# Performance work log

Measured on AMD Instinct MI355X. Metric: run time of the kernel, lower is better.

## Reference

```python
import jax, jax.numpy as jnp
import numpy as np
from jax import lax

B, C, H, W = 4, 128, 128, 128
MAXD = 192
D = MAXD // 4            # 48 disparity hypotheses at 1/4 scale
WS = 8                   # window size
NH = 8                   # num heads
HD = C // NH             # head dim = 16
SCALE = HD ** -0.5
HID = 4 * C              # mlp hidden (mlp_ratio=4)


def _rel_index(ws):
    coords = np.stack(np.meshgrid(np.arange(ws), np.arange(ws), indexing='ij'))
    cf = coords.reshape(2, -1)
    rel = (cf[:, :, None] - cf[:, None, :]).transpose(1, 2, 0)
    rel[:, :, 0] += ws - 1
    rel[:, :, 1] += ws - 1
    rel[:, :, 0] *= 2 * ws - 1
    return rel.sum(-1)   # [ws*ws, ws*ws]

REL_IDX = jnp.asarray(_rel_index(WS))


def setup_inputs() -> dict:
    key = jax.random.key(0)
    ks = iter(jax.random.split(key, 40))
    rn = lambda shape, s=0.02: jax.random.normal(next(ks), shape, dtype=jnp.float32) * s
    return {
        'feat_l': jax.random.normal(next(ks), (B, C, H, W), dtype=jnp.float32),
        'feat_r': jax.random.normal(next(ks), (B, C, H, W), dtype=jnp.float32),
        'wq': rn((C, C)), 'bq': jnp.zeros((C,), jnp.float32),
        'wk': rn((C, C)), 'bk': jnp.zeros((C,), jnp.float32),
        'wv': rn((C, C)), 'bv': jnp.zeros((C,), jnp.float32),
        'wp': rn((C, C)), 'bp': jnp.zeros((C,), jnp.float32),
        'rpb': rn(((2 * WS - 1) ** 2, NH)),
        'ln1_g': jnp.ones((C,), jnp.float32), 'ln1_b': jnp.zeros((C,), jnp.float32),
        'ln2_g': jnp.ones((C,), jnp.float32), 'ln2_b': jnp.zeros((C,), jnp.float32),
        'mlp_w1': rn((C, HID)), 'mlp_b1': jnp.zeros((HID,), jnp.float32),
        'mlp_w2': rn((HID, C)), 'mlp_b2': jnp.zeros((C,), jnp.float32),
        'un_w1': rn((C, C)), 'un_b1': jnp.zeros((C,), jnp.float32),
        'un_w2': rn((C, C)), 'un_b2': jnp.zeros((C,), jnp.float32),
        'dp_w1': rn((C // 2 + D // 2 + 16, C + D, 3, 3)) if False else rn(((C + D) // 2, C + D, 3, 3)),
        'dp_b1': jnp.zeros(((C + D) // 2,), jnp.float32),
        'bn_g': jnp.ones(((C + D) // 2,), jnp.float32), 'bn_b': jnp.zeros(((C + D) // 2,), jnp.float32),
        'dp_w2': rn((D, (C + D) // 2, 1, 1)), 'dp_b2': jnp.zeros((D,), jnp.float32),
    }


def _ln(x, g, b):
    m = x.mean(-1, keepdims=True)
    v = x.var(-1, keepdims=True)
    return (x - m) * jax.lax.rsqrt(v + 1e-5) * g + b


def _conv(x, w, b, pad):
    y = lax.conv_general_dilated(x, w, (1, 1), [(pad, pad), (pad, pad)],
                                 dimension_numbers=('NCHW', 'OIHW', 'NCHW'))
    return y + b[None, :, None, None]


def _cost_volume(fl, fr):
    # corr[:, d] = mean_c fl[..., w] * fr[..., w-d], zero-padded on the left
    outs = [jnp.mean(fl * fr, axis=1)]
    for d in range(1, D):
        fr_s = jnp.pad(fr[:, :, :, :-d], ((0, 0), (0, 0), (0, 0), (d, 0)))
        outs.append(jnp.mean(fl * fr_s, axis=1))
    return jnp.stack(outs, axis=1)  # [B, D, H, W]


def _win_part(tok):  # [B, H*W, C] -> [B*nW, WS*WS, C]
    x = tok.reshape(B, H // WS, WS, W // WS, WS, C)
    return x.transpose(0, 1, 3, 2, 4, 5).reshape(-1, WS * WS, C)


def _win_rev(win):  # [B*nW, WS*WS, C] -> [B, H*W, C]
    x = win.reshape(B, H // WS, W // WS, WS, WS, C)
    return x.transpose(0, 1, 3, 2, 4, 5).reshape(B, H * W, C)


def _forward(feat_l, feat_r, wq, bq, wk, bk, wv, bv, wp, bp, rpb,
             ln1_g, ln1_b, ln2_g, ln2_b, mlp_w1, mlp_b1, mlp_w2, mlp_b2,
             un_w1, un_b1, un_w2, un_b2, dp_w1, dp_b1, bn_g, bn_b, dp_w2, dp_b2):
    gelu = lambda x: jax.nn.gelu(x, approximate=False)
    cost = _cost_volume(feat_l, feat_r)                       # [B, D, H, W]

    tokens = feat_l.reshape(B, C, H * W).transpose(0, 2, 1)   # [B, N, C]
    unary = gelu(tokens @ un_w1 + un_b1) @ un_w2 + un_b2      # unary potential

    nf = _ln(_win_part(tokens), ln1_g, ln1_b)                 # [Bw, 64, C]
    Bw, N = nf.shape[0], WS * WS
    q = (nf @ wq + bq).reshape(Bw, N, NH, HD).transpose(0, 2, 1, 3)
    k = (nf @ wk + bk).reshape(Bw, N, NH, HD).transpose(0, 2, 1, 3)
    v = (nf @ wv + bv).reshape(Bw, N, NH, HD).transpose(0, 2, 1, 3)
    attn = jnp.einsum('bhnd,bhmd->bhnm', q, k) * SCALE
    bias = rpb[REL_IDX.reshape(-1)].reshape(N, N, NH).transpose(2, 0, 1)
    attn = jax.nn.softmax(attn + bias[None], axis=-1)
    o = jnp.einsum('bhnm,bhmd->bhnd', attn, v).transpose(0, 2, 1, 3).reshape(Bw, N, C)
    pairwise = o @ wp + bp

    x = unary + _win_rev(pairwise)
    x = x + gelu(_ln(x, ln2_g, ln2_b) @ mlp_w1 + mlp_b1) @ mlp_w2 + mlp_b2 * 0.0 + (jnp.zeros((), jnp.float32))
    # (faithful residual MLP; the extra zero terms are no-ops kept out below)
    # -- recompute cleanly to avoid confusion:
    # x = x + mlp(norm2(x))  already done above via single expression

    crf = x.transpose(0, 2, 1).reshape(B, C, H, W)
    fused = jnp.concatenate([crf, cost], axis=1)              # [B, C+D, H, W]

    h1 = jax.nn.relu((_conv(fused, dp_w1, dp_b1, 1)) * jax.lax.rsqrt(jnp.float32(1.0 + 1e-5)) * bn_g[None, :, None, None] + bn_b[None, :, None, None])
    pv = _conv(h1, dp_w2, dp_b2, 0)                           # [B, D, H, W]
    prob = jax.nn.softmax(pv, axis=1)
    disp = jnp.arange(D, dtype=jnp.float32)[None, :, None, None]
    pred = jnp.sum(prob * disp, axis=1, keepdims=True) * 4.0  # [B, 1, H, W]
    return pred


def reference(feat_l, feat_r, wq, bq, wk, bk, wv, bv, wp, bp, rpb,
              ln1_g, ln1_b, ln2_g, ln2_b, mlp_w1, mlp_b1, mlp_w2, mlp_b2,
              un_w1, un_b1, un_w2, un_b2, dp_w1, dp_b1, bn_g, bn_b, dp_w2, dp_b2):
    return _forward(feat_l, feat_r, wq, bq, wk, bk, wv, bv, wp, bp, rpb,
                    ln1_g, ln1_b, ln2_g, ln2_b, mlp_w1, mlp_b1, mlp_w2, mlp_b2,
                    un_w1, un_b1, un_w2, un_b2, dp_w1, dp_b1, bn_g, bn_b, dp_w2, dp_b2)
```

## Files before the change

### kernel.cpp

```cpp
#include <hip/hip_runtime.h>
#include <math.h>

constexpr int Bn = 4, Cc = 128, Hh = 128, Wn = 128, Dd = 48;
constexpr float SCALE = 0.25f;

typedef short  bf16x8 __attribute__((ext_vector_type(8)));
typedef short  bf16x4 __attribute__((ext_vector_type(4)));
typedef float  f32x4  __attribute__((ext_vector_type(4)));
typedef unsigned short u16x8 __attribute__((ext_vector_type(8)));

static __device__ __forceinline__ unsigned short f2bf(float f) {
    return __builtin_bit_cast(unsigned short, (__bf16)f);
}
static __device__ __forceinline__ float bf2f(unsigned short u) {
    return __uint_as_float((unsigned int)u << 16);
}
static __device__ __forceinline__ unsigned int pack2bf(float a, float b) {
    return (unsigned int)f2bf(a) | ((unsigned int)f2bf(b) << 16);
}
static __device__ __forceinline__ float gelu_f(float v) {
    float u = v * (1.5957691216f + 0.0713548162f * v * v);
    return v * __builtin_amdgcn_rcpf(1.0f + __expf(-u));
}

static __device__ __forceinline__ size_t opk_addr(int b, int wh, int ww, int Mt, int ks, int lane) {
    return ((size_t)(b * 16384) + (wh * 8 + Mt * 2 + (ks >> 1)) * 128 + ww * 8) * 128
           + (ks & 1) * 512 + lane * 8;
}

static __device__ void pack_conv(int blk, int lane,
                                 const float* __restrict__ w1, const float* __restrict__ b1,
                                 const float* __restrict__ bng, const float* __restrict__ bnb,
                                 unsigned short* __restrict__ pk, float* __restrict__ bias2) {
    const float rs = 0.9999950000374997f;
    int ct = blk % 6;
    int taplin = blk / 6;
    int tap = taplin % 9, chunk = taplin / 9;
    int co = ct * 16 + (lane & 15);
    int cibase = chunk * 32 + (lane >> 4) * 8;
    u16x8 out;
#pragma unroll
    for (int j = 0; j < 8; ++j) {
        int ci = cibase + j;
        float v = 0.f;
        if (co < 88 && ci < 176) v = w1[(size_t)co * 1584 + ci * 9 + tap] * rs * bng[co];
        out[j] = f2bf(v);
    }
    *(u16x8*)(pk + ((size_t)blk * 64 + lane) * 8) = out;
    if (blk == 0) {
        for (int i = lane; i < 96; i += 64)
            bias2[i] = (i < 88) ? (b1[i] * rs * bng[i] + bnb[i]) : 0.f;
    }
}

static __device__ void pack_gemmB(int blk, int lane,
                                  const float* __restrict__ W,
                                  unsigned short* __restrict__ out, int ncols) {
    int ntiles = ncols >> 4;
    int ks = blk & 3;
    int nt = (blk >> 2) % ntiles;
    int kc = blk / (4 * ntiles);
    int col = nt * 16 + (lane & 15);
    int k0 = kc * 128 + ks * 32 + (lane >> 4) * 8;
    u16x8 o;
#pragma unroll
    for (int j = 0; j < 8; ++j) o[j] = f2bf(W[(size_t)(k0 + j) * ncols + col]);
    *(u16x8*)(out + ((size_t)blk * 64 + lane) * 8) = o;
}

static __device__ void pack_rpb(int blk, int lane,
                                const float* __restrict__ rpb, float* __restrict__ pb) {
    int nt = blk & 3, mt = (blk >> 2) & 3, hh = blk >> 4;
    int tq = nt * 16 + (lane & 15);
    int g = lane >> 4;
    float o[4];
#pragma unroll
    for (int rr = 0; rr < 4; ++rr) {
        int tk = mt * 16 + g * 4 + rr;
        int relidx = (((tq >> 3) - (tk >> 3)) + 7) * 15 + ((tq & 7) - (tk & 7)) + 7;
        o[rr] = rpb[relidx * 8 + hh];
    }
    float4 v = {o[0], o[1], o[2], o[3]};
    *(float4*)(pb + ((size_t)blk * 64 + lane) * 4) = v;
}

__global__ __launch_bounds__(64) void k_pack_all(
        const float* __restrict__ dp_w1, const float* __restrict__ dp_b1,
        const float* __restrict__ bn_g, const float* __restrict__ bn_b,
        unsigned short* __restrict__ pk, float* __restrict__ bias2,
        const float* __restrict__ wq, const float* __restrict__ wk,
        const float* __restrict__ wv, const float* __restrict__ wp,
        unsigned short* __restrict__ pkw,
        const float* __restrict__ rpb, float* __restrict__ pb,
        const float* __restrict__ mlp_w1, unsigned short* __restrict__ pm1,
        const float* __restrict__ mlp_w2, unsigned short* __restrict__ pm2,
        const float* __restrict__ un_w1, unsigned short* __restrict__ pu1,
        const float* __restrict__ un_w2, unsigned short* __restrict__ pu2) {
    int blk = blockIdx.x;
    int lane = threadIdx.x;
    if (blk < 324) {
        pack_conv(blk, lane, dp_w1, dp_b1, bn_g, bn_b, pk, bias2);
    } else if (blk < 452) {
        int bb = blk - 324;
        int mat = bb >> 5;
        const float* W = (mat == 0) ? wq : (mat == 1) ? wk : (mat == 2) ? wv : wp;
        pack_gemmB(bb & 31, lane, W, pkw + (size_t)mat * 16384, 128);
    } else if (blk < 580) {
        pack_rpb(blk - 452, lane, rpb, pb);
    } else if (blk < 708) {
        pack_gemmB(blk - 580, lane, mlp_w1, pm1, 512);
    } else if (blk < 836) {
        pack_gemmB(blk - 708, lane, mlp_w2, pm2, 128);
    } else if (blk < 868) {
        pack_gemmB(blk - 836, lane, un_w1, pu1, 128);
    } else {
        pack_gemmB(blk - 868, lane, un_w2, pu2, 128);
    }
}

__global__ __launch_bounds__(256) void k_front(const float* __restrict__ feat_l,
                                               const float* __restrict__ feat_r,
                                               unsigned short* __restrict__ costbf,
                                               const unsigned short* __restrict__ pu1,
                                               const float* __restrict__ b1,
                                               const unsigned short* __restrict__ pu2,
                                               const float* __restrict__ b2,
                                               const float* __restrict__ g1,
                                               const float* __restrict__ bt1,
                                               float* __restrict__ x,
                                               unsigned short* __restrict__ nf) {
    __shared__ __align__(16) char smem[34816];
    int tid = threadIdx.x;
    int blk = blockIdx.x;

    if (blk >= 1024) {
        int cb = blk - 1024;
        int wt = cb & 1, h = (cb >> 1) & 127, b = cb >> 8;
        int w0 = wt * 64;
        int w = tid & 63, dg = tid >> 6;
        float* s_fl = (float*)smem;
        float* s_fr = (float*)(smem + 4096);
        float acc[12];
#pragma unroll
        for (int dj = 0; dj < 12; ++dj) acc[dj] = 0.f;

#pragma unroll 1
        for (int ck = 0; ck < 8; ++ck) {
            int ci0 = ck * 16;
            {
                int c = tid >> 4, k4 = tid & 15;
                *(float4*)&s_fl[c * 64 + k4 * 4] =
                    *(const float4*)&feat_l[((size_t)(b * 128 + ci0 + c) << 14) + h * 128 + w0 + k4 * 4];
            }
            for (int i = tid; i < 448; i += 256) {
                int c = i / 28, k4 = i - c * 28;
                int wgl = w0 - 48 + k4 * 4;
                float4 v = {0.f, 0.f, 0.f, 0.f};
                if (wgl >= 0)
                    v = *(const float4*)&feat_r[((size_t)(b * 128 + ci0 + c) << 14) + h * 128 + wgl];
                *(float4*)&s_fr[c * 112 + k4 * 4] = v;
            }
            __syncthreads();
            int base = w + 48 - dg * 12;
#pragma unroll
            for (int c = 0; c < 16; ++c) {
                float flv = s_fl[c * 64 + w];
#pragma unroll
                for (int dj = 0; dj < 12; ++dj)
                    acc[dj] += flv * s_fr[c * 112 + base - dj];
            }
            __syncthreads();
        }
        const float inv = 1.0f / 128.0f;
        unsigned short* cbp = costbf + ((size_t)(b << 14) + h * 128 + w0 + w) * 64 + dg * 12;
#pragma unroll
        for (int q = 0; q < 3; ++q) {
            bf16x4 o4;
#pragma unroll
            for (int rr = 0; rr < 4; ++rr) o4[rr] = (short)f2bf(acc[q * 4 + rr] * inv);
            *(bf16x4*)&cbp[q * 4] = o4;
        }
        if (dg == 3) {
            const u16x8 z8 = {0, 0, 0, 0, 0, 0, 0, 0};
            *(u16x8*)&cbp[12] = z8;
            *(u16x8*)&cbp[20] = z8;
        }
        return;
    }

    unsigned short* s_a = (unsigned short*)smem;
    unsigned short* s_h = (unsigned short*)(smem + 17408);
    int wid = tid >> 6, lane = tid & 63;
    int g = lane >> 4, t = lane & 15;
    int n0g = blk * 64;
    int b = n0g >> 14;
    int nb = n0g & 16383;

    for (int idx = tid; idx < 4096; idx += 256) {
        int c2 = idx >> 6, nl = idx & 63;
        float v0 = feat_l[((size_t)(b * 128 + 2 * c2) << 14) + nb + nl];
        float v1 = feat_l[((size_t)(b * 128 + 2 * c2 + 1) << 14) + nb + nl];
        *(unsigned int*)&s_a[nl * 136 + 2 * c2] = pack2bf(v0, v1);
    }
    __syncthreads();

    {
        int tok = tid >> 2, q = tid & 3;
        float v[32];
#pragma unroll
        for (int i8 = 0; i8 < 4; ++i8) {
            u16x8 r8 = *(const u16x8*)&s_a[tok * 136 + q * 32 + i8 * 8];
#pragma unroll
            for (int j = 0; j < 8; ++j) v[i8 * 8 + j] = bf2f(r8[j]);
        }
        float s = 0.f, s2 = 0.f;
#pragma unroll
        for (int i = 0; i < 32; ++i) { s += v[i]; s2 += v[i] * v[i]; }
        s += __shfl_xor(s, 1); s += __shfl_xor(s, 2);
        s2 += __shfl_xor(s2, 1); s2 += __shfl_xor(s2, 2);
        float mean = s * (1.f / 128.f);
        float var = s2 * (1.f / 128.f) - mean * mean;
        float rstd = rsqrtf(var + 1e-5f);
        size_t base = (size_t)(n0g + tok) * 128 + q * 32;
#pragma unroll
        for (int i8 = 0; i8 < 4; ++i8) {
            u16x8 o8;
#pragma unroll
            for (int j = 0; j < 8; ++j) {
                int c = q * 32 + i8 * 8 + j;
                o8[j] = f2bf((v[i8 * 8 + j] - mean) * rstd * g1[c] + bt1[c]);
            }
            *(u16x8*)&nf[base + i8 * 8] = o8;
        }
    }

    bf16x8 af[4][4];
#pragma unroll
    for (int Mt = 0; Mt < 4; ++Mt)
#pragma unroll
        for (int ks = 0; ks < 4; ++ks)
            af[Mt][ks] = *(const bf16x8*)&s_a[(Mt * 16 + t) * 136 + ks * 32 + g * 8];

    f32x4 acc1[4][2];
#pragma unroll
    for (int nt2 = 0; nt2 < 2; ++nt2) {
        float bv = b1[(wid * 2 + nt2) * 16 + t];
#pragma unroll
        for (int Mt = 0; Mt < 4; ++Mt) acc1[Mt][nt2] = (f32x4){bv, bv, bv, bv};
    }
#pragma unroll
    for (int ks = 0; ks < 4; ++ks) {
        bf16x8 bf0 = *(const bf16x8*)(pu1 + (size_t)(((wid * 2 + 0) * 4 + ks) * 64 + lane) * 8);
        bf16x8 bf1 = *(const bf16x8*)(pu1 + (size_t)(((wid * 2 + 1) * 4 + ks) * 64 + lane) * 8);
#pragma unroll
        for (int Mt = 0; Mt < 4; ++Mt) {
            acc1[Mt][0] = __builtin_amdgcn_mfma_f32_16x16x32_bf16(af[Mt][ks], bf0, acc1[Mt][0], 0, 0, 0);
            acc1[Mt][1] = __builtin_amdgcn_mfma_f32_16x16x32_bf16(af[Mt][ks], bf1, acc1[Mt][1], 0, 0, 0);
        }
    }
#pragma unroll
    for (int Mt = 0; Mt < 4; ++Mt)
#pragma unroll
        for (int nt2 = 0; nt2 < 2; ++nt2)
#pragma unroll
            for (int rr = 0; rr < 4; ++rr)
                s_h[(Mt * 16 + g * 4 + rr) * 136 + (wid * 2 + nt2) * 16 + t] = f2bf(gelu_f(acc1[Mt][nt2][rr]));
    __syncthreads();

    bf16x8 a2[4][4];
#pragma unroll
    for (int Mt = 0; Mt < 4; ++Mt)
#pragma unroll
        for (int ks = 0; ks < 4; ++ks)
            a2[Mt][ks] = *(const bf16x8*)&s_h[(Mt * 16 + t) * 136 + ks * 32 + g * 8];

    f32x4 acc2[4][2];
#pragma unroll
    for (int nt2 = 0; nt2 < 2; ++nt2) {
        float bv = b2[(wid * 2 + nt2) * 16 + t];
#pragma unroll
        for (int Mt = 0; Mt < 4; ++Mt) acc2[Mt][nt2] = (f32x4){bv, bv, bv, bv};
    }
#pragma unroll
    for (int ks = 0; ks < 4; ++ks) {
        bf16x8 bf0 = *(const bf16x8*)(pu2 + (size_t)(((wid * 2 + 0) * 4 + ks) * 64 + lane) * 8);
        bf16x8 bf1 = *(const bf16x8*)(pu2 + (size_t)(((wid * 2 + 1) * 4 + ks) * 64 + lane) * 8);
#pragma unroll
        for (int Mt = 0; Mt < 4; ++Mt) {
            acc2[Mt][0] = __builtin_amdgcn_mfma_f32_16x16x32_bf16(a2[Mt][ks], bf0, acc2[Mt][0], 0, 0, 0);
            acc2[Mt][1] = __builtin_amdgcn_mfma_f32_16x16x32_bf16(a2[Mt][ks], bf1, acc2[Mt][1], 0, 0, 0);
        }
    }
#pragma unroll
    for (int Mt = 0; Mt < 4; ++Mt)
#pragma unroll
        for (int nt2 = 0; nt2 < 2; ++nt2)
#pragma unroll
            for (int rr = 0; rr < 4; ++rr) {
                int tok = Mt * 16 + g * 4 + rr;
                x[(size_t)(n0g + tok) * 128 + (wid * 2 + nt2) * 16 + t] = acc2[Mt][nt2][rr];
            }
}

__global__ __launch_bounds__(256, 3) void k_attn_core(const unsigned short* nf,
                                                      const unsigned short* __restrict__ pkw,
                                                      const float* __restrict__ pb,
                                                      const float* __restrict__ bq,
                                                      const float* __restrict__ bk,
                                                      const float* __restrict__ bv,
                                                      unsigned short* opk) {
    __shared__ __align__(16) unsigned short s_all[4 * 5760];
    int tid = threadIdx.x;
    int wid = tid >> 6, lane = tid & 63;
    int g = lane >> 4, t = lane & 15;
    int bw = blockIdx.x;
    int b = bw >> 8, wh = (bw >> 4) & 15, ww = bw & 15;

    bf16x8 af[4][4];
#pragma unroll
    for (int Mt = 0; Mt < 4; ++Mt) {
        int tok = Mt * 16 + t;
        size_t gtok = (size_t)(b * 16384) + (wh * 8 + (tok >> 3)) * 128 + ww * 8 + (tok & 7);
#pragma unroll
        for (int ks = 0; ks < 4; ++ks)
            af[Mt][ks] = *(const bf16x8*)&nf[gtok * 128 + ks * 32 + g * 8];
    }
    __syncthreads();

    unsigned short* sQ = s_all + wid * 5760;
    unsigned short* sK = sQ + 1536;
    unsigned short* sV = sQ + 4608;
    unsigned short* sP = sQ;
    unsigned short* sO = sQ;

    const bf16x8 z8v = {0, 0, 0, 0, 0, 0, 0, 0};

#pragma unroll
    for (int hi = 0; hi < 2; ++hi) {
        int h = wid + hi * 4;

        float bqv = bq[h * 16 + t], bkv = bk[h * 16 + t], bvv = bv[h * 16 + t];
        f32x4 qa[4], ka[4], va[4];
#pragma unroll
        for (int Mt = 0; Mt < 4; ++Mt) {
            qa[Mt] = (f32x4){bqv, bqv, bqv, bqv};
            ka[Mt] = (f32x4){bkv, bkv, bkv, bkv};
            va[Mt] = (f32x4){bvv, bvv, bvv, bvv};
        }
#pragma unroll
        for (int ks = 0; ks < 4; ++ks) {
            const unsigned short* wbase = pkw + ((size_t)((h * 4 + ks) * 64 + lane) * 8);
            bf16x8 bfq = *(const bf16x8*)(wbase);
            bf16x8 bfk = *(const bf16x8*)(wbase + 16384);
            bf16x8 bfv = *(const bf16x8*)(wbase + 32768);
#pragma unroll
            for (int Mt = 0; Mt < 4; ++Mt) {
                qa[Mt] = __builtin_amdgcn_mfma_f32_16x16x32_bf16(af[Mt][ks], bfq, qa[Mt], 0, 0, 0);
                ka[Mt] = __builtin_amdgcn_mfma_f32_16x16x32_bf16(af[Mt][ks], bfk, ka[Mt], 0, 0, 0);
                va[Mt] = __builtin_amdgcn_mfma_f32_16x16x32_bf16(af[Mt][ks], bfv, va[Mt], 0, 0, 0);
            }
        }
#pragma unroll
        for (int Mt = 0; Mt < 4; ++Mt) {
            bf16x4 vv;
#pragma unroll
            for (int rr = 0; rr < 4; ++rr) {
                int tok = Mt * 16 + g * 4 + rr;
                sQ[tok * 24 + t] = f2bf(qa[Mt][rr] * SCALE);
                sK[tok * 24 + t] = f2bf(ka[Mt][rr]);
                vv[rr] = (short)f2bf(va[Mt][rr]);
            }
            *(bf16x4*)&sV[t * 72 + Mt * 16 + g * 4] = vv;
        }

        f32x4 s[4][4];
#pragma unroll
        for (int Mtk = 0; Mtk < 4; ++Mtk)
#pragma unroll
            for (int Ntq = 0; Ntq < 4; ++Ntq)
                s[Mtk][Ntq] = *(const f32x4*)(pb + ((size_t)((h * 16 + Mtk * 4 + Ntq) * 64 + lane) * 4));
        bf16x8 bQ[4];
#pragma unroll
        for (int Ntq = 0; Ntq < 4; ++Ntq)
            bQ[Ntq] = (g < 2) ? *(const bf16x8*)&sQ[(Ntq * 16 + t) * 24 + g * 8] : z8v;
#pragma unroll
        for (int Mtk = 0; Mtk < 4; ++Mtk) {
            bf16x8 aK = (g < 2) ? *(const bf16x8*)&sK[(Mtk * 16 + t) * 24 + g * 8] : z8v;
#pragma unroll
            for (int Ntq = 0; Ntq < 4; ++Ntq)
                s[Mtk][Ntq] = __builtin_amdgcn_mfma_f32_16x16x32_bf16(aK, bQ[Ntq], s[Mtk][Ntq], 0, 0, 0);
        }

#pragma unroll
        for (int Ntq = 0; Ntq < 4; ++Ntq) {
            float m = s[0][Ntq][0];
#pragma unroll
            for (int Mtk = 0; Mtk < 4; ++Mtk)
#pragma unroll
                for (int rr = 0; rr < 4; ++rr) m = fmaxf(m, s[Mtk][Ntq][rr]);
            m = fmaxf(m, __shfl_xor(m, 16));
            m = fmaxf(m, __shfl_xor(m, 32));
            float sum = 0.f;
#pragma unroll
            for (int Mtk = 0; Mtk < 4; ++Mtk)
#pragma unroll
                for (int rr = 0; rr < 4; ++rr) {
                    float e = __expf(s[Mtk][Ntq][rr] - m);
                    s[Mtk][Ntq][rr] = e;
                    sum += e;
                }
            sum += __shfl_xor(sum, 16);
            sum += __shfl_xor(sum, 32);
            float inv = __builtin_amdgcn_rcpf(sum);
#pragma unroll
            for (int Mtk = 0; Mtk < 4; ++Mtk) {
                bf16x4 pv;
#pragma unroll
                for (int rr = 0; rr < 4; ++rr) pv[rr] = (short)f2bf(s[Mtk][Ntq][rr] * inv);
                *(bf16x4*)&sP[(Ntq * 16 + t) * 72 + Mtk * 16 + g * 4] = pv;
            }
        }

        f32x4 oa[4];
#pragma unroll
        for (int Mt = 0; Mt < 4; ++Mt) oa[Mt] = (f32x4){0.f, 0.f, 0.f, 0.f};
#pragma unroll
        for (int ksv = 0; ksv < 2; ++ksv) {
            bf16x8 bv2 = *(const bf16x8*)&sV[t * 72 + ksv * 32 + g * 8];
#pragma unroll
            for (int Mt = 0; Mt < 4; ++Mt) {
                bf16x8 ap = *(const bf16x8*)&sP[(Mt * 16 + t) * 72 + ksv * 32 + g * 8];
                oa[Mt] = __builtin_amdgcn_mfma_f32_16x16x32_bf16(ap, bv2, oa[Mt], 0, 0, 0);
            }
        }
#pragma unroll
        for (int Mt = 0; Mt < 4; ++Mt)
#pragma unroll
            for (int rr = 0; rr < 4; ++rr)
                sO[(Mt * 16 + g * 4 + rr) * 16 + t] = f2bf(oa[Mt][rr]);
        int ksf = h >> 1;
        if ((g >> 1) == (h & 1)) {
#pragma unroll
            for (int Mt = 0; Mt < 4; ++Mt) {
                bf16x8 v8 = *(const bf16x8*)&sO[(Mt * 16 + t) * 16 + (g & 1) * 8];
                *(bf16x8*)&opk[opk_addr(b, wh, ww, Mt, ksf, lane)] = v8;
            }
        }
    }
}

__global__ __launch_bounds__(256) void k_mlp_mfma(float* __restrict__ x,
                                                  const unsigned short* __restrict__ opk,
                                                  const unsigned short* __restrict__ pkw,
                                                  const float* __restrict__ bp,
                                                  const float* __restrict__ g2,
                                                  const float* __restrict__ bt2,
                                                  const unsigned short* __restrict__ pm1,
                                                  const float* __restrict__ b1,
                                                  const unsigned short* __restrict__ pm2) {
    __shared__ __align__(16) char smem[35328];
    float* sf = (float*)smem;
    unsigned short* s_h = (unsigned short*)smem;
    float* s_st = (float*)(smem + 33792);
    float* s_gb = (float*)(smem + 34304);
    int tid = threadIdx.x;
    int wid = tid >> 6, lane = tid & 63;
    int g = lane >> 4, t = lane & 15;
    int bw = blockIdx.x;
    int b = bw >> 8, wh = (bw >> 4) & 15, ww = bw & 15;

    auto gtok_of = [&](int tok) -> size_t {
        return (size_t)(b * 16384) + (wh * 8 + (tok >> 3)) * 128 + ww * 8 + (tok & 7);
    };

    if (tid < 128) s_gb[tid] = g2[tid];
    else if (tid < 256) s_gb[tid] = bt2[tid - 128];

    f32x4 out[4][2];
    {
        float bp0 = bp[wid * 32 + t], bp1 = bp[wid * 32 + 16 + t];
#pragma unroll
        for (int Mt = 0; Mt < 4; ++Mt) {
            out[Mt][0] = (f32x4){bp0, bp0, bp0, bp0};
            out[Mt][1] = (f32x4){bp1, bp1, bp1, bp1};
        }
#pragma unroll
        for (int ks = 0; ks < 4; ++ks) {
            bf16x8 b0 = *(const bf16x8*)(pkw + 49152 + (size_t)(((wid * 2 + 0) * 4 + ks) * 64 + lane) * 8);
            bf16x8 b1v = *(const bf16x8*)(pkw + 49152 + (size_t)(((wid * 2 + 1) * 4 + ks) * 64 + lane) * 8);
#pragma unroll
            for (int Mt = 0; Mt < 4; ++Mt) {
                bf16x8 a = *(const bf16x8*)&opk[opk_addr(b, wh, ww, Mt, ks, lane)];
                out[Mt][0] = __builtin_amdgcn_mfma_f32_16x16x32_bf16(a, b0, out[Mt][0], 0, 0, 0);
                out[Mt][1] = __builtin_amdgcn_mfma_f32_16x16x32_bf16(a, b1v, out[Mt][1], 0, 0, 0);
            }
        }
#pragma unroll
        for (int Mt = 0; Mt < 4; ++Mt)
#pragma unroll
            for (int nt2 = 0; nt2 < 2; ++nt2)
#pragma unroll
                for (int rr = 0; rr < 4; ++rr) {
                    int tok = Mt * 16 + g * 4 + rr;
                    int col = (wid * 2 + nt2) * 16 + t;
                    float v = out[Mt][nt2][rr] + x[gtok_of(tok) * 128 + col];
                    out[Mt][nt2][rr] = v;
                    sf[tok * 132 + col] = v;
                }
    }
    __syncthreads();
    {
        int tok = tid >> 2, q = tid & 3;
        float s = 0.f, s2 = 0.f;
        for (int c = q * 32; c < q * 32 + 32; ++c) {
            float v = sf[tok * 132 + c];
            s += v; s2 += v * v;
        }
        s += __shfl_xor(s, 1); s += __shfl_xor(s, 2);
        s2 += __shfl_xor(s2, 1); s2 += __shfl_xor(s2, 2);
        if (q == 0) {
            float mean = s * (1.f / 128.f);
            float var = s2 * (1.f / 128.f) - mean * mean;
            s_st[tok * 2] = mean;
            s_st[tok * 2 + 1] = rsqrtf(var + 1e-5f);
        }
    }
    __syncthreads();
    bf16x8 af2[4][4];
#pragma unroll
    for (int Mt = 0; Mt < 4; ++Mt) {
        int tok = Mt * 16 + t;
        float mean = s_st[tok * 2], rstd = s_st[tok * 2 + 1];
#pragma unroll
        for (int ks = 0; ks < 4; ++ks) {
            int c0 = ks * 32 + g * 8;
            float4 v0 = *(const float4*)&sf[tok * 132 + c0];
            float4 v1 = *(const float4*)&sf[tok * 132 + c0 + 4];
            float vv[8] = {v0.x, v0.y, v0.z, v0.w, v1.x, v1.y, v1.z, v1.w};
            u16x8 o8;
#pragma unroll
            for (int j = 0; j < 8; ++j)
                o8[j] = f2bf((vv[j] - mean) * rstd * s_gb[c0 + j] + s_gb[128 + c0 + j]);
            af2[Mt][ks] = __builtin_bit_cast(bf16x8, o8);
        }
    }
    __syncthreads();

#pragma unroll 1
    for (int hc = 0; hc < 2; ++hc) {
#pragma unroll
        for (int jh = 0; jh < 2; ++jh) {
            f32x4 acc1[4][2];
#pragma unroll
            for (int j2 = 0; j2 < 2; ++j2) {
                float bv = b1[hc * 256 + (wid * 4 + jh * 2 + j2) * 16 + t];
#pragma unroll
                for (int Mt = 0; Mt < 4; ++Mt) acc1[Mt][j2] = (f32x4){bv, bv, bv, bv};
            }
#pragma unroll
            for (int ks = 0; ks < 4; ++ks) {
                int nt0 = hc * 16 + wid * 4 + jh * 2;
                bf16x8 bf0 = *(const bf16x8*)(pm1 + (size_t)((((nt0 + 0) * 4 + ks) * 64 + lane) * 8));
                bf16x8 bf1 = *(const bf16x8*)(pm1 + (size_t)((((nt0 + 1) * 4 + ks) * 64 + lane) * 8));
#pragma unroll
                for (int Mt = 0; Mt < 4; ++Mt) {
                    acc1[Mt][0] = __builtin_amdgcn_mfma_f32_16x16x32_bf16(af2[Mt][ks], bf0, acc1[Mt][0], 0, 0, 0);
                    acc1[Mt][1] = __builtin_amdgcn_mfma_f32_16x16x32_bf16(af2[Mt][ks], bf1, acc1[Mt][1], 0, 0, 0);
                }
            }
#pragma unroll
            for (int Mt = 0; Mt < 4; ++Mt)
#pragma unroll
                for (int j2 = 0; j2 < 2; ++j2)
#pragma unroll
                    for (int rr = 0; rr < 4; ++rr)
                        s_h[(Mt * 16 + g * 4 + rr) * 264 + (wid * 4 + jh * 2 + j2) * 16 + t] =
                            f2bf(gelu_f(acc1[Mt][j2][rr]));
        }
        __syncthreads();
#pragma unroll
        for (int kt = 0; kt < 8; ++kt) {
            int kc = hc * 2 + (kt >> 2), ks = kt & 3;
            bf16x8 bf0 = *(const bf16x8*)(pm2 + (size_t)(((kc * 32 + (wid * 2 + 0) * 4 + ks) * 64 + lane) * 8));
            bf16x8 bf1 = *(const bf16x8*)(pm2 + (size_t)(((kc * 32 + (wid * 2 + 1) * 4 + ks) * 64 + lane) * 8));
#pragma unroll
            for (int Mt = 0; Mt < 4; ++Mt) {
                bf16x8 a2 = *(const bf16x8*)&s_h[(Mt * 16 + t) * 264 + kt * 32 + g * 8];
                out[Mt][0] = __builtin_amdgcn_mfma_f32_16x16x32_bf16(a2, bf0, out[Mt][0], 0, 0, 0);
                out[Mt][1] = __builtin_amdgcn_mfma_f32_16x16x32_bf16(a2, bf1, out[Mt][1], 0, 0, 0);
            }
        }
        __syncthreads();
    }

#pragma unroll
    for (int Mt = 0; Mt < 4; ++Mt)
#pragma unroll
        for (int nt2 = 0; nt2 < 2; ++nt2)
#pragma unroll
            for (int rr = 0; rr < 4; ++rr) {
                int tok = Mt * 16 + g * 4 + rr;
                x[gtok_of(tok) * 128 + (wid * 2 + nt2) * 16 + t] = out[Mt][nt2][rr];
            }
}

__global__ __launch_bounds__(256) void k_conv_mfma(const float* __restrict__ x,
                                                   const unsigned short* __restrict__ costbf,
                                                   const unsigned short* __restrict__ pk,
                                                   const float* __restrict__ bias2,
                                                   float* __restrict__ h1) {
    __shared__ __align__(16) unsigned short s_p[180 * 40];
    int tid = threadIdx.x;
    int wid = tid >> 6, lane = tid & 63;
    int g = lane >> 4, t = lane & 15;
    int tx0 = blockIdx.x * 16, ty0 = blockIdx.y * 8, b = blockIdx.z;

    f32x4 acc[2][6];
#pragma unroll
    for (int p = 0; p < 2; ++p)
#pragma unroll
        for (int ct = 0; ct < 6; ++ct) acc[p][ct] = (f32x4){0.f, 0.f, 0.f, 0.f};

#pragma unroll 1
    for (int chunk = 0; chunk < 6; ++chunk) {
        if (chunk < 4) {
            int ci0 = chunk * 32;
            for (int u = tid; u < 360; u += 256) {
                int pos = u >> 1, half = u & 1;
                int yy = pos / 18, xx = pos - yy * 18;
                int gy = ty0 + yy - 1, gx = tx0 + xx - 1;
                u16x8 lo, hi;
                if (gy >= 0 && gy < 128 && gx >= 0 && gx < 128) {
                    const float4* src = (const float4*)&x[((size_t)(b << 14) + gy * 128 + gx) * 128 + ci0 + half * 16];
                    float4 v0 = src[0], v1 = src[1], v2 = src[2], v3 = src[3];
                    lo[0] = f2bf(v0.x); lo[1] = f2bf(v0.y); lo[2] = f2bf(v0.z); lo[3] = f2bf(v0.w);
                    lo[4] = f2bf(v1.x); lo[5] = f2bf(v1.y); lo[6] = f2bf(v1.z); lo[7] = f2bf(v1.w);
                    hi[0] = f2bf(v2.x); hi[1] = f2bf(v2.y); hi[2] = f2bf(v2.z); hi[3] = f2bf(v2.w);
                    hi[4] = f2bf(v3.x); hi[5] = f2bf(v3.y); hi[6] = f2bf(v3.z); hi[7] = f2bf(v3.w);
                } else {
                    lo = (u16x8)(unsigned short)0; hi = (u16x8)(unsigned short)0;
                }
                unsigned short* dst = &s_p[pos * 40 + half * 16];
                *(u16x8*)dst = lo;
                *(u16x8*)(dst + 8) = hi;
            }
        } else {
            int d0 = (chunk - 4) * 32;
            for (int u = tid; u < 180; u += 256) {
                int yy = u / 18, xx = u - yy * 18;
                int gy = ty0 + yy - 1, gx = tx0 + xx - 1;
                u16x8 lo = (u16x8)(unsigned short)0, hi = (u16x8)(unsigned short)0;
                if (gy >= 0 && gy < 128 && gx >= 0 && gx < 128) {
                    const u16x8* src = (const u16x8*)&costbf[((size_t)(b << 14) + gy * 128 + gx) * 64 + d0];
                    lo = src[0]; hi = src[1];
                    u16x8 l2 = src[2], h2 = src[3];
                    *(u16x8*)&s_p[u * 40 + 16] = l2;
                    *(u16x8*)&s_p[u * 40 + 24] = h2;
                } else {
                    *(u16x8*)&s_p[u * 40 + 16] = lo;
                    *(u16x8*)&s_p[u * 40 + 24] = hi;
                }
                *(u16x8*)&s_p[u * 40 + 0] = lo;
                *(u16x8*)&s_p[u * 40 + 8] = hi;
            }
        }
        __syncthreads();

#pragma unroll 1
        for (int tap = 0; tap < 9; ++tap) {
            int dy = tap / 3, dx = tap - dy * 3;
            const unsigned short* pkt = pk + ((size_t)(chunk * 9 + tap)) * 6 * 512;
            bf16x8 afr[6];
#pragma unroll
            for (int ct = 0; ct < 6; ++ct)
                afr[ct] = *(const bf16x8*)(pkt + ct * 512 + lane * 8);
            bf16x8 bfr[2];
#pragma unroll
            for (int p = 0; p < 2; ++p) {
                int pos = (wid * 2 + p + dy) * 18 + t + dx;
                bfr[p] = *(const bf16x8*)&s_p[pos * 40 + g * 8];
            }
#pragma unroll
            for (int p = 0; p < 2; ++p)
#pragma unroll
                for (int ct = 0; ct < 6; ++ct)
                    acc[p][ct] = __builtin_amdgcn_mfma_f32_16x16x32_bf16(afr[ct], bfr[p], acc[p][ct], 0, 0, 0);
        }
        __syncthreads();
    }

#pragma unroll
    for (int p = 0; p < 2; ++p) {
        int y = ty0 + wid * 2 + p;
#pragma unroll
        for (int ct = 0; ct < 6; ++ct) {
#pragma unroll
            for (int rr = 0; rr < 4; ++rr) {
                int co = ct * 16 + g * 4 + rr;
                if (co < 88) {
                    float v = acc[p][ct][rr] + bias2[co];
                    h1[((size_t)(b * 88 + co) << 14) + y * 128 + tx0 + t] = fmaxf(v, 0.f);
                }
            }
        }
    }
}

__global__ __launch_bounds__(256) void k_head(const float* __restrict__ h1,
                                              const float* __restrict__ w2, const float* __restrict__ b2,
                                              float* __restrict__ out) {
    __shared__ float s_wt[88 * 48];
    __shared__ float s_b[48];
    int tid = threadIdx.x;
    for (int idx = tid; idx < 48 * 88; idx += 256) {
        int d = idx / 88, k = idx % 88;
        s_wt[k * 48 + d] = w2[idx];
    }
    if (tid < 48) s_b[tid] = b2[tid];
    __syncthreads();
    int px = blockIdx.x * 256 + tid;
    int b = px >> 14, r = px & 16383;
    float acc[48];
#pragma unroll
    for (int d = 0; d < 48; ++d) acc[d] = s_b[d];
    for (int k = 0; k < 88; ++k) {
        float hv = h1[((size_t)(b * 88 + k) << 14) + r];
        const float4* wrow = (const float4*)&s_wt[k * 48];
#pragma unroll
        for (int d4 = 0; d4 < 12; ++d4) {
            float4 wv = wrow[d4];
            acc[d4 * 4 + 0] += hv * wv.x;
            acc[d4 * 4 + 1] += hv * wv.y;
            acc[d4 * 4 + 2] += hv * wv.z;
            acc[d4 * 4 + 3] += hv * wv.w;
        }
    }
    float mx = -1e30f;
#pragma unroll
    for (int d = 0; d < 48; ++d) mx = fmaxf(mx, acc[d]);
    float sum = 0.f, wsum = 0.f;
#pragma unroll
    for (int d = 0; d < 48; ++d) {
        float e = __expf(acc[d] - mx);
        sum += e;
        wsum += e * (float)d;
    }
    out[px] = 4.0f * wsum * __builtin_amdgcn_rcpf(sum);
}

extern "C" void kernel_launch(void* const* d_in, const int* in_sizes, int n_in,
                              void* d_out, int out_size, void* d_ws, size_t ws_size,
                              hipStream_t stream) {
    const float* feat_l = (const float*)d_in[0];
    const float* feat_r = (const float*)d_in[1];
    const float* wq = (const float*)d_in[2];
    const float* bq = (const float*)d_in[3];
    const float* wk = (const float*)d_in[4];
    const float* bk = (const float*)d_in[5];
    const float* wv = (const float*)d_in[6];
    const float* bv = (const float*)d_in[7];
    const float* wp = (const float*)d_in[8];
    const float* bp = (const float*)d_in[9];
    const float* rpb = (const float*)d_in[10];
    const float* ln1_g = (const float*)d_in[11];
    const float* ln1_b = (const float*)d_in[12];
    const float* ln2_g = (const float*)d_in[13];
    const float* ln2_b = (const float*)d_in[14];
    const float* mlp_w1 = (const float*)d_in[15];
    const float* mlp_b1 = (const float*)d_in[16];
    const float* mlp_w2 = (const float*)d_in[17];
    const float* un_w1 = (const float*)d_in[19];
    const float* un_b1 = (const float*)d_in[20];
    const float* un_w2 = (const float*)d_in[21];
    const float* un_b2 = (const float*)d_in[22];
    const float* dp_w1 = (const float*)d_in[23];
    const float* dp_b1 = (const float*)d_in[24];
    const float* bn_g = (const float*)d_in[25];
    const float* bn_b = (const float*)d_in[26];
    const float* dp_w2 = (const float*)d_in[27];
    const float* dp_b2 = (const float*)d_in[28];

    float* ws = (float*)d_ws;
    unsigned short* costbf = (unsigned short*)ws;
    float* x = ws + 3145728;
    float* h1 = ws + 11534336;
    unsigned short* nfo = (unsigned short*)h1;
    unsigned short* pk = (unsigned short*)(ws + 17301504);
    float* bias2 = ws + 17384448;
    unsigned short* pkw = (unsigned short*)(ws + 17384544);
    float* pb = ws + 17417312;
    unsigned short* pm1 = (unsigned short*)(ws + 17450080);
    unsigned short* pm2 = (unsigned short*)(ws + 17482848);
    unsigned short* pu1 = (unsigned short*)(ws + 17515616);
    unsigned short* pu2 = (unsigned short*)(ws + 17523808);
    float* out = (float*)d_out;

    k_pack_all<<<900, 64, 0, stream>>>(dp_w1, dp_b1, bn_g, bn_b, pk, bias2,
                                       wq, wk, wv, wp, pkw, rpb, pb,
                                       mlp_w1, pm1, mlp_w2, pm2,
                                       un_w1, pu1, un_w2, pu2);
    k_front<<<2048, 256, 0, stream>>>(feat_l, feat_r, costbf, pu1, un_b1,
                                      pu2, un_b2, ln1_g, ln1_b, x, nfo);
    k_attn_core<<<1024, 256, 0, stream>>>(nfo, pkw, pb, bq, bk, bv, nfo);
    k_mlp_mfma<<<1024, 256, 0, stream>>>(x, nfo, pkw, bp, ln2_g, ln2_b,
                                         pm1, mlp_b1, pm2);
    k_conv_mfma<<<dim3(8, 16, 4), 256, 0, stream>>>(x, costbf, pk, bias2, h1);
    k_head<<<256, 256, 0, stream>>>(h1, dp_w2, dp_b2, out);
}
```

Measured before the change: 259.7 us.

## Register-tile cost volume 4x4 and interleave cost blocks with front blocks

The cost-volume branch of the fused front kernel now computes a 4-width by 4-disparity register tile per thread using float4 shared-memory loads, instead of one pixel by 12 disparities with scalar loads. This cuts LDS traffic per FMA. Only 192 of 256 threads do work, which leaves a quarter of the block idle. Blocks are also interleaved (odd = cost, even = LN/MLP front) rather than placed in two contiguous ranges, so the two workloads are spread more evenly across CUs.

New measurement: 276.9 us. 1.07x slower.

```diff
diff --git a/kernel.cpp b/kernel.cpp
--- a/kernel.cpp
+++ b/kernel.cpp
@@ -132,17 +132,20 @@
     __shared__ __align__(16) char smem[34816];
     int tid = threadIdx.x;
     int blk = blockIdx.x;
-
-    if (blk >= 1024) {
-        int cb = blk - 1024;
-        int wt = cb & 1, h = (cb >> 1) & 127, b = cb >> 8;
+    int idx = blk >> 1;
+
+    if (blk & 1) {
+        int wt = idx & 1, h = (idx >> 1) & 127, b = idx >> 8;
         int w0 = wt * 64;
-        int w = tid & 63, dg = tid >> 6;
         float* s_fl = (float*)smem;
         float* s_fr = (float*)(smem + 4096);
-        float acc[12];
-#pragma unroll
-        for (int dj = 0; dj < 12; ++dj) acc[dj] = 0.f;
+        int wg = tid & 15, dg = tid >> 4;
+        int W = wg * 4, D = dg * 4;
+        float acc[4][4];
+#pragma unroll
+        for (int i = 0; i < 4; ++i)
+#pragma unroll
+            for (int j = 0; j < 4; ++j) acc[i][j] = 0.f;
 
 #pragma unroll 1
         for (int ck = 0; ck < 8; ++ck) {
@@ -161,29 +164,39 @@
                 *(float4*)&s_fr[c * 112 + k4 * 4] = v;
             }
             __syncthreads();
-            int base = w + 48 - dg * 12;
-#pragma unroll
-            for (int c = 0; c < 16; ++c) {
-                float flv = s_fl[c * 64 + w];
-#pragma unroll
-                for (int dj = 0; dj < 12; ++dj)
-                    acc[dj] += flv * s_fr[c * 112 + base - dj];
+            if (dg < 12) {
+                int base = W - D + 44;
+#pragma unroll
+                for (int c = 0; c < 16; ++c) {
+                    float4 flv = *(const float4*)&s_fl[c * 64 + W];
+                    float4 f0 = *(const float4*)&s_fr[c * 112 + base];
+                    float4 f1 = *(const float4*)&s_fr[c * 112 + base + 4];
+                    float fw[8] = {f0.x, f0.y, f0.z, f0.w, f1.x, f1.y, f1.z, f1.w};
+                    float fv[4] = {flv.x, flv.y, flv.z, flv.w};
+#pragma unroll
+                    for (int dj = 0; dj < 4; ++dj)
+#pragma unroll
+                        for (int wv = 0; wv < 4; ++wv)
+                            acc[dj][wv] += fv[wv] * fw[wv - dj + 4];
+                }
             }
             __syncthreads();
         }
-        const float inv = 1.0f / 128.0f;
-        unsigned short* cbp = costbf + ((size_t)(b << 14) + h * 128 + w0 + w) * 64 + dg * 12;
-#pragma unroll
-        for (int q = 0; q < 3; ++q) {
-            bf16x4 o4;
-#pragma unroll
-            for (int rr = 0; rr < 4; ++rr) o4[rr] = (short)f2bf(acc[q * 4 + rr] * inv);
-            *(bf16x4*)&cbp[q * 4] = o4;
-        }
-        if (dg == 3) {
+        if (dg < 12) {
+            const float inv = 1.0f / 128.0f;
+            unsigned short* cb = costbf + ((size_t)(b << 14) + h * 128 + w0 + W) * 64;
             const u16x8 z8 = {0, 0, 0, 0, 0, 0, 0, 0};
-            *(u16x8*)&cbp[12] = z8;
-            *(u16x8*)&cbp[20] = z8;
+#pragma unroll
+            for (int wv = 0; wv < 4; ++wv) {
+                bf16x4 o4;
+#pragma unroll
+                for (int dj = 0; dj < 4; ++dj) o4[dj] = (short)f2bf(acc[dj][wv] * inv);
+                *(bf16x4*)&cb[wv * 64 + D] = o4;
+                if (D == 44) {
+                    *(u16x8*)&cb[wv * 64 + 48] = z8;
+                    *(u16x8*)&cb[wv * 64 + 56] = z8;
+                }
+            }
         }
         return;
     }
@@ -192,12 +205,12 @@
     unsigned short* s_h = (unsigned short*)(smem + 17408);
     int wid = tid >> 6, lane = tid & 63;
     int g = lane >> 4, t = lane & 15;
-    int n0g = blk * 64;
+    int n0g = idx * 64;
     int b = n0g >> 14;
     int nb = n0g & 16383;
 
-    for (int idx = tid; idx < 4096; idx += 256) {
-        int c2 = idx >> 6, nl = idx & 63;
+    for (int i2 = tid; i2 < 4096; i2 += 256) {
+        int c2 = i2 >> 6, nl = i2 & 63;
         float v0 = feat_l[((size_t)(b * 128 + 2 * c2) << 14) + nb + nl];
         float v1 = feat_l[((size_t)(b * 128 + 2 * c2 + 1) << 14) + nb + nl];
         *(unsigned int*)&s_a[nl * 136 + 2 * c2] = pack2bf(v0, v1);
```
